# Kernel tuning notes

Measured on AMD Instinct MI355X. Metric: run time of the kernel, lower is better.

## Reference

```python
import jax, jax.numpy as jnp
import numpy as np

D_MODEL, N_HEADS, D_FF = 1024, 16, 4096
D_K = D_MODEL // N_HEADS
EPS = 1e-5


def setup_inputs() -> dict:
    key = jax.random.key(0)
    ks = jax.random.split(key, 16)
    s = 0.02
    p = {
        'x': jax.random.normal(ks[0], (2, 2048, D_MODEL), jnp.float32),
        'Wq': jax.random.normal(ks[1], (D_MODEL, D_MODEL), jnp.float32) * s,
        'bq': jnp.zeros((D_MODEL,), jnp.float32),
        'Wk': jax.random.normal(ks[2], (D_MODEL, D_MODEL), jnp.float32) * s,
        'bk': jnp.zeros((D_MODEL,), jnp.float32),
        'Wv': jax.random.normal(ks[3], (D_MODEL, D_MODEL), jnp.float32) * s,
        'bv': jnp.zeros((D_MODEL,), jnp.float32),
        'Wo': jax.random.normal(ks[4], (D_MODEL, D_MODEL), jnp.float32) * s,
        'bo': jnp.zeros((D_MODEL,), jnp.float32),
        'g1': jnp.ones((D_MODEL,), jnp.float32),
        'b1': jnp.zeros((D_MODEL,), jnp.float32),
        'W1': jax.random.normal(ks[5], (D_MODEL, D_FF), jnp.float32) * s,
        'bf1': jnp.zeros((D_FF,), jnp.float32),
        'W2': jax.random.normal(ks[6], (D_FF, D_MODEL), jnp.float32) * s,
        'bf2': jnp.zeros((D_MODEL,), jnp.float32),
        'g2': jnp.ones((D_MODEL,), jnp.float32),
        'b2': jnp.zeros((D_MODEL,), jnp.float32),
    }
    return p


def _layernorm(x, g, b):
    mu = jnp.mean(x, axis=-1, keepdims=True)
    var = jnp.var(x, axis=-1, keepdims=True)
    return (x - mu) * jax.lax.rsqrt(var + EPS) * g + b


def reference(x, Wq, bq, Wk, bk, Wv, bv, Wo, bo, g1, b1, W1, bf1, W2, bf2, g2, b2):
    B, S, _ = x.shape
    # project and split heads -> [B, H, S, d_k]
    def heads(y):
        return y.reshape(B, S, N_HEADS, D_K).transpose(0, 2, 1, 3)
    Q = heads(x @ Wq + bq)
    K = heads(x @ Wk + bk)
    V = heads(x @ Wv + bv)
    scores = jnp.einsum('bhqd,bhkd->bhqk', Q, K) / np.sqrt(D_K).astype(np.float32)
    attn = jax.nn.softmax(scores, axis=-1)  # dropout = identity (eval)
    ctx = jnp.einsum('bhqk,bhkd->bhqd', attn, V)
    ctx = ctx.transpose(0, 2, 1, 3).reshape(B, S, D_MODEL)
    attn_out = ctx @ Wo + bo
    h = _layernorm(x + attn_out, g1, b1)
    ff = (jax.nn.gelu(h @ W1 + bf1, approximate=False)) @ W2 + bf2
    out = _layernorm(h + ff, g2, b2)
    return out, attn
```

## Files before the change

kernel.cpp:

```cpp
#include <hip/hip_runtime.h>
#include <stdint.h>

#define SEQ 2048
#define BATCH 2
#define NH 16
#define DKH 64
#define DM 1024
#define DFF 4096
#define MTOT (BATCH*SEQ)

typedef __attribute__((ext_vector_type(8))) short bf16x8;
typedef __attribute__((ext_vector_type(4))) float f32x4;

__device__ __forceinline__ unsigned short f2bf(float f) {
  union { float f; unsigned u; } c; c.f = f;
  return (unsigned short)((c.u + 0x7fffu + ((c.u >> 16) & 1u)) >> 16);
}

__device__ __forceinline__ void gload_lds16(const void* g, void* l) {
  __builtin_amdgcn_global_load_lds((__attribute__((address_space(1))) unsigned int*)g,
                                   (__attribute__((address_space(3))) unsigned int*)l,
                                   16, 0, 0);
}


__global__ __launch_bounds__(256) void conv_bf16(const float* __restrict__ X,
                                                 unsigned short* __restrict__ O, int n) {
  const int i = blockIdx.x * 256 + threadIdx.x;
  const int idx = i * 4;
  if (idx >= n) return;
  const float4 f = *(const float4*)(X + idx);
  ushort4 u; u.x = f2bf(f.x); u.y = f2bf(f.y); u.z = f2bf(f.z); u.w = f2bf(f.w);
  *(ushort4*)(O + idx) = u;
}

__global__ __launch_bounds__(256) void trans_conv(const float* __restrict__ W,
                                                  unsigned short* __restrict__ Wt,
                                                  int K, int N) {
  __shared__ float t[32][33];
  const int n0 = blockIdx.x * 32, k0 = blockIdx.y * 32;
  const int tx = threadIdx.x & 31, ty = threadIdx.x >> 5;
#pragma unroll
  for (int i = 0; i < 4; ++i)
    t[ty + i * 8][tx] = W[(long)(k0 + ty + i * 8) * N + n0 + tx];
  __syncthreads();
#pragma unroll
  for (int i = 0; i < 4; ++i)
    Wt[(long)(n0 + ty + i * 8) * K + k0 + tx] = f2bf(t[tx][ty + i * 8]);
}

__global__ __launch_bounds__(256) void concat3(const float* __restrict__ a,
                                               const float* __restrict__ b,
                                               const float* __restrict__ c,
                                               float* __restrict__ o) {
  const int i = blockIdx.x * 256 + threadIdx.x;
  o[i] = i < 1024 ? a[i] : (i < 2048 ? b[i - 1024] : c[i - 2048]);
}

template <int EPI, int KS>
__global__ __launch_bounds__(256 * KS) void gemm_bt(
    const unsigned short* __restrict__ A, const unsigned short* __restrict__ Bt,
    float* __restrict__ Cf, unsigned short* __restrict__ Cbf,
    const float* __restrict__ bias, const float* __restrict__ resid,
    unsigned short* __restrict__ Vt,
    int M, int N, int K, int lda, int ldb, int ldc) {
  (void)M; (void)N;
  __shared__ unsigned short ldsAB[KS * 2 * 128 * 64];

  const int tid = threadIdx.x;
  const int ws = tid >> 8;
  const int t2 = tid & 255;
  const int lane = tid & 63;
  const int w4 = (tid >> 6) & 3;
  const int quad = lane >> 4, l16 = lane & 15;
  const int wm = (w4 >> 1) * 64, wn = (w4 & 1) * 64;
  const long tileM = (long)blockIdx.x * 128;
  const long tileN = (long)blockIdx.y * 128;

  unsigned short* ldsA = ldsAB + ws * 16384;
  unsigned short* ldsB = ldsA + 8192;
  const int kLen = K / KS;
  const int kBase = ws * kLen;

  const unsigned short* aS[4];
  const unsigned short* bS[4];
  int dOff[4];
#pragma unroll
  for (int it = 0; it < 4; ++it) {
    const int c = it * 256 + t2;
    const int slab = c >> 9, row = (c >> 2) & 127, q = c & 3;
    aS[it] = A  + (tileM + row) * (long)lda + kBase + slab * 32 + q * 8;
    bS[it] = Bt + (tileN + row) * (long)ldb + kBase + slab * 32 + q * 8;
    dOff[it] = c * 8;
  }

  f32x4 acc[4][4];
#pragma unroll
  for (int i = 0; i < 4; ++i)
#pragma unroll
    for (int j = 0; j < 4; ++j)
#pragma unroll
      for (int r = 0; r < 4; ++r) acc[i][j][r] = 0.f;

  for (int k0 = 0; k0 < kLen; k0 += 64) {
    __syncthreads();
#pragma unroll
    for (int it = 0; it < 4; ++it) {
      gload_lds16(aS[it] + k0, ldsA + dOff[it]);
      gload_lds16(bS[it] + k0, ldsB + dOff[it]);
    }
    __syncthreads();
#pragma unroll
    for (int s = 0; s < 2; ++s) {
      bf16x8 aF[4], bF[4];
#pragma unroll
      for (int i = 0; i < 4; ++i)
        aF[i] = *(const bf16x8*)&ldsA[(s * 128 + wm + i * 16 + l16) * 32 + quad * 8];
#pragma unroll
      for (int j = 0; j < 4; ++j)
        bF[j] = *(const bf16x8*)&ldsB[(s * 128 + wn + j * 16 + l16) * 32 + quad * 8];
#pragma unroll
      for (int i = 0; i < 4; ++i)
#pragma unroll
        for (int j = 0; j < 4; ++j)
          acc[i][j] = __builtin_amdgcn_mfma_f32_16x16x32_bf16(aF[i], bF[j], acc[i][j], 0, 0, 0);
    }
  }

  if constexpr (KS == 2) {
    __syncthreads();
    float* ldsF = (float*)ldsAB;
    if (ws == 1) {
#pragma unroll
      for (int i = 0; i < 4; ++i)
#pragma unroll
        for (int j = 0; j < 4; ++j)
#pragma unroll
          for (int r = 0; r < 4; ++r)
            ldsF[(wm + i * 16 + quad * 4 + r) * 128 + wn + j * 16 + l16] = acc[i][j][r];
    }
    __syncthreads();
    if (ws == 1) return;
#pragma unroll
    for (int i = 0; i < 4; ++i)
#pragma unroll
      for (int j = 0; j < 4; ++j)
#pragma unroll
        for (int r = 0; r < 4; ++r)
          acc[i][j][r] += ldsF[(wm + i * 16 + quad * 4 + r) * 128 + wn + j * 16 + l16];
  }

#pragma unroll
  for (int i = 0; i < 4; ++i) {
    const long mb = tileM + wm + i * 16 + quad * 4;
#pragma unroll
    for (int j = 0; j < 4; ++j) {
      const long n = tileN + wn + j * 16 + l16;
      const float bv = bias[n];
      if (EPI == 4) {
        if (n < 2048) {
          unsigned short* dst = Cbf + (n >> 10) * ((long)MTOT * DM);
          const int col = (int)n & 1023;
#pragma unroll
          for (int r = 0; r < 4; ++r)
            dst[(mb + r) * DM + col] = f2bf(acc[i][j][r] + bv);
        } else {
          const int nn = (int)n - 2048;
          const int bb2 = (int)(mb >> 11), s = (int)(mb & 2047);
          const int zz = bb2 * 16 + (nn >> 6);
          ushort4 u;
          u.x = f2bf(acc[i][j][0] + bv); u.y = f2bf(acc[i][j][1] + bv);
          u.z = f2bf(acc[i][j][2] + bv); u.w = f2bf(acc[i][j][3] + bv);
          *(ushort4*)&Vt[((long)zz * DKH + (nn & 63)) * SEQ + s] = u;
        }
      } else {
#pragma unroll
        for (int r = 0; r < 4; ++r) {
          const long m = mb + r;
          const long idx = m * ldc + n;
          const float v = acc[i][j][r];
          if (EPI == 0) {
            Cbf[idx] = f2bf(v + bv);
          } else if (EPI == 2) {
            Cf[idx] = v + bv + resid[idx];
          } else {
            const float tt = v + bv;
            Cbf[idx] = f2bf(0.5f * tt * (1.f + erff(tt * 0.70710678118654752f)));
          }
        }
      }
    }
  }
}

__device__ __forceinline__ void stage_k128(const unsigned short* __restrict__ gbase,
                                           unsigned short* lds, int tid) {
#pragma unroll
  for (int it = 0; it < 4; ++it) {
    const int c = it * 256 + tid;
    const int slab = c >> 9, row = (c >> 2) & 127, q = c & 3;
    gload_lds16(gbase + (long)row * DM + slab * 32 + q * 8, lds + c * 8);
  }
}
__device__ __forceinline__ void stage_v64(const unsigned short* __restrict__ gbase,
                                          unsigned short* lds, int tid) {
#pragma unroll
  for (int it = 0; it < 4; ++it) {
    const int c = it * 256 + tid;
    const int slab = c >> 8, row = (c >> 2) & 63, q = c & 3;
    gload_lds16(gbase + (long)row * SEQ + slab * 32 + q * 8, lds + c * 8);
  }
}

__global__ __launch_bounds__(256) void attn_all(const unsigned short* __restrict__ Qbf,
                                                const unsigned short* __restrict__ Kbf,
                                                const unsigned short* __restrict__ Vt,
                                                float* __restrict__ attn,
                                                unsigned short* __restrict__ Ctx) {
  const int z = blockIdx.z, b = z >> 4, h = z & 15;
  const int m0 = blockIdx.x * 128;

  __shared__ unsigned short ldsQ[2 * 128 * 32];
  __shared__ unsigned short ldsK[2 * 128 * 32];
  __shared__ unsigned short ldsV[4 * 64 * 32];
  __shared__ unsigned short ldsP[4 * 128 * 32];

  const int tid = threadIdx.x;
  const int lane = tid & 63, wave = tid >> 6;
  const int quad = lane >> 4, l16 = lane & 15;
  const int wm = (wave >> 1) * 64, wn = (wave & 1) * 64;
  const int wn2 = (wave & 1) * 32;

  const unsigned short* Qbase = Qbf + ((long)(b * SEQ + m0)) * DM + h * DKH;
  const unsigned short* Kz = Kbf + ((long)b * SEQ) * DM + h * DKH;
  const unsigned short* Vz = Vt + (long)z * DKH * SEQ;

  stage_k128(Qbase, ldsQ, tid);
  stage_k128(Kz, ldsK, tid);
  __syncthreads();

  bf16x8 qF[2][4];
#pragma unroll
  for (int s = 0; s < 2; ++s)
#pragma unroll
    for (int i = 0; i < 4; ++i)
      qF[s][i] = *(const bf16x8*)&ldsQ[(s * 128 + wm + i * 16 + l16) * 32 + quad * 8];
  __syncthreads();

  float rm[4][4], rl[4][4];
#pragma unroll
  for (int i = 0; i < 4; ++i)
#pragma unroll
    for (int r = 0; r < 4; ++r) { rm[i][r] = -1e30f; rl[i][r] = 0.f; }

  for (int n = 0; n < 16; ++n) {
    if (n) __syncthreads();
    if (n < 15) stage_k128(Kz + (long)(n + 1) * 128 * DM, (n & 1) ? ldsK : ldsQ, tid);
    const unsigned short* kc = (n & 1) ? ldsQ : ldsK;

    f32x4 acc[4][4];
#pragma unroll
    for (int i = 0; i < 4; ++i)
#pragma unroll
      for (int j = 0; j < 4; ++j)
#pragma unroll
        for (int r = 0; r < 4; ++r) acc[i][j][r] = 0.f;
#pragma unroll
    for (int s = 0; s < 2; ++s) {
      bf16x8 bF[4];
#pragma unroll
      for (int j = 0; j < 4; ++j)
        bF[j] = *(const bf16x8*)&kc[(s * 128 + wn + j * 16 + l16) * 32 + quad * 8];
#pragma unroll
      for (int i = 0; i < 4; ++i)
#pragma unroll
        for (int j = 0; j < 4; ++j)
          acc[i][j] = __builtin_amdgcn_mfma_f32_16x16x32_bf16(qF[s][i], bF[j], acc[i][j], 0, 0, 0);
    }
#pragma unroll
    for (int i = 0; i < 4; ++i)
#pragma unroll
      for (int r = 0; r < 4; ++r) {
        const float v0 = acc[i][0][r] * 0.125f, v1 = acc[i][1][r] * 0.125f;
        const float v2 = acc[i][2][r] * 0.125f, v3 = acc[i][3][r] * 0.125f;
        const float tm = fmaxf(fmaxf(v0, v1), fmaxf(v2, v3));
        const float mn = fmaxf(rm[i][r], tm);
        rl[i][r] = rl[i][r] * __expf(rm[i][r] - mn) +
                   __expf(v0 - mn) + __expf(v1 - mn) + __expf(v2 - mn) + __expf(v3 - mn);
        rm[i][r] = mn;
      }
  }

#pragma unroll
  for (int i = 0; i < 4; ++i)
#pragma unroll
    for (int r = 0; r < 4; ++r) {
      float m = rm[i][r], l = rl[i][r];
#pragma unroll
      for (int o = 1; o < 16; o <<= 1) {
        const float om = __shfl_xor(m, o), ol = __shfl_xor(l, o);
        const float mn = fmaxf(m, om);
        l = l * __expf(m - mn) + ol * __expf(om - mn);
        m = mn;
      }
      rm[i][r] = m; rl[i][r] = l;
    }

  float2* sm = (float2*)ldsP;
  if (l16 == 0) {
#pragma unroll
    for (int i = 0; i < 4; ++i)
#pragma unroll
      for (int r = 0; r < 4; ++r)
        sm[wave * 64 + i * 16 + quad * 4 + r] = make_float2(rm[i][r], rl[i][r]);
  }
  __syncthreads();
  float sM[4][4], sI[4][4];
#pragma unroll
  for (int i = 0; i < 4; ++i)
#pragma unroll
    for (int r = 0; r < 4; ++r) {
      const int rr = i * 16 + quad * 4 + r;
      const float2 A = sm[(wave & ~1) * 64 + rr];
      const float2 B = sm[((wave & ~1) + 1) * 64 + rr];
      const float M = fmaxf(A.x, B.x);
      const float Z = A.y * __expf(A.x - M) + B.y * __expf(B.x - M);
      sM[i][r] = M; sI[i][r] = 1.f / Z;
    }

  f32x4 acc_o[4][2];
#pragma unroll
  for (int i = 0; i < 4; ++i)
#pragma unroll
    for (int j = 0; j < 2; ++j)
#pragma unroll
      for (int r = 0; r < 4; ++r) acc_o[i][j][r] = 0.f;

  stage_k128(Kz, ldsK, tid);
  __syncthreads();

  for (int n = 0; n < 16; ++n) {
    if (n) __syncthreads();
    if (n < 15) stage_k128(Kz + (long)(n + 1) * 128 * DM, (n & 1) ? ldsK : ldsQ, tid);
    stage_v64(Vz + n * 128, ldsV, tid);
    const unsigned short* kc = (n & 1) ? ldsQ : ldsK;

    f32x4 acc[4][4];
#pragma unroll
    for (int i = 0; i < 4; ++i)
#pragma unroll
      for (int j = 0; j < 4; ++j)
#pragma unroll
        for (int r = 0; r < 4; ++r) acc[i][j][r] = 0.f;
    __builtin_amdgcn_s_setprio(1);
#pragma unroll
    for (int s = 0; s < 2; ++s) {
      bf16x8 bF[4];
#pragma unroll
      for (int j = 0; j < 4; ++j)
        bF[j] = *(const bf16x8*)&kc[(s * 128 + wn + j * 16 + l16) * 32 + quad * 8];
#pragma unroll
      for (int i = 0; i < 4; ++i)
#pragma unroll
        for (int j = 0; j < 4; ++j)
          acc[i][j] = __builtin_amdgcn_mfma_f32_16x16x32_bf16(qF[s][i], bF[j], acc[i][j], 0, 0, 0);
    }
    __builtin_amdgcn_s_setprio(0);

    float* attnBase = attn + (long)z * SEQ * SEQ + (long)m0 * SEQ + n * 128;
#pragma unroll
    for (int i = 0; i < 4; ++i)
#pragma unroll
      for (int r = 0; r < 4; ++r) {
        const int rowl = wm + i * 16 + quad * 4 + r;
        const float M = sM[i][r], I = sI[i][r];
#pragma unroll
        for (int j = 0; j < 4; ++j) {
          const int col = wn + j * 16 + l16;
          const float p = __expf(acc[i][j][r] * 0.125f - M) * I;
          attnBase[(long)rowl * SEQ + col] = p;
          ldsP[((col >> 5) * 128 + rowl) * 32 + (col & 31)] = f2bf(p);
        }
      }
    __syncthreads();

    __builtin_amdgcn_s_setprio(1);
#pragma unroll
    for (int slab = 0; slab < 4; ++slab) {
      bf16x8 aF[4], bF[2];
#pragma unroll
      for (int i = 0; i < 4; ++i)
        aF[i] = *(const bf16x8*)&ldsP[(slab * 128 + wm + i * 16 + l16) * 32 + quad * 8];
#pragma unroll
      for (int j = 0; j < 2; ++j)
        bF[j] = *(const bf16x8*)&ldsV[(slab * 64 + wn2 + j * 16 + l16) * 32 + quad * 8];
#pragma unroll
      for (int i = 0; i < 4; ++i)
#pragma unroll
        for (int j = 0; j < 2; ++j)
          acc_o[i][j] = __builtin_amdgcn_mfma_f32_16x16x32_bf16(aF[i], bF[j], acc_o[i][j], 0, 0, 0);
    }
    __builtin_amdgcn_s_setprio(0);
  }

#pragma unroll
  for (int i = 0; i < 4; ++i)
#pragma unroll
    for (int j = 0; j < 2; ++j) {
      const int d = h * DKH + wn2 + j * 16 + l16;
#pragma unroll
      for (int r = 0; r < 4; ++r) {
        const long m = (long)b * SEQ + m0 + wm + i * 16 + quad * 4 + r;
        Ctx[m * DM + d] = f2bf(acc_o[i][j][r]);
      }
    }
}

__global__ __launch_bounds__(256) void layernorm_row(const float* __restrict__ Y,
                                                     const float* __restrict__ g,
                                                     const float* __restrict__ bb,
                                                     float* __restrict__ outF,
                                                     unsigned short* __restrict__ outBf) {
  const long row = blockIdx.x;
  const float* p = Y + row * DM;
  const int tid = threadIdx.x;
  const float4 v = *(const float4*)(p + tid * 4);
  float s = v.x + v.y + v.z + v.w;
  float ss = v.x * v.x + v.y * v.y + v.z * v.z + v.w * v.w;
#pragma unroll
  for (int o = 32; o > 0; o >>= 1) { s += __shfl_xor(s, o); ss += __shfl_xor(ss, o); }
  __shared__ float rs[4], rss[4];
  if ((tid & 63) == 0) { rs[tid >> 6] = s; rss[tid >> 6] = ss; }
  __syncthreads();
  s = rs[0] + rs[1] + rs[2] + rs[3];
  ss = rss[0] + rss[1] + rss[2] + rss[3];
  const float mu = s * (1.f / DM);
  const float var = ss * (1.f / DM) - mu * mu;
  const float rstd = rsqrtf(var + 1e-5f);
  const float4 gv = *(const float4*)(g + tid * 4);
  const float4 bv = *(const float4*)(bb + tid * 4);
  float4 o;
  o.x = (v.x - mu) * rstd * gv.x + bv.x;
  o.y = (v.y - mu) * rstd * gv.y + bv.y;
  o.z = (v.z - mu) * rstd * gv.z + bv.z;
  o.w = (v.w - mu) * rstd * gv.w + bv.w;
  *(float4*)(outF + row * DM + tid * 4) = o;
  if (outBf) {
    ushort4 u; u.x = f2bf(o.x); u.y = f2bf(o.y); u.z = f2bf(o.z); u.w = f2bf(o.w);
    *(ushort4*)(outBf + row * DM + tid * 4) = u;
  }
}

extern "C" void kernel_launch(void* const* d_in, const int* in_sizes, int n_in,
                              void* d_out, int out_size, void* d_ws, size_t ws_size,
                              hipStream_t stream) {
  (void)in_sizes; (void)n_in; (void)out_size; (void)ws_size;
  const float* x  = (const float*)d_in[0];
  const float* Wq = (const float*)d_in[1];
  const float* bq = (const float*)d_in[2];
  const float* Wk = (const float*)d_in[3];
  const float* bk = (const float*)d_in[4];
  const float* Wv = (const float*)d_in[5];
  const float* bv = (const float*)d_in[6];
  const float* Wo = (const float*)d_in[7];
  const float* bo = (const float*)d_in[8];
  const float* g1 = (const float*)d_in[9];
  const float* b1 = (const float*)d_in[10];
  const float* W1 = (const float*)d_in[11];
  const float* bf1 = (const float*)d_in[12];
  const float* W2 = (const float*)d_in[13];
  const float* bf2 = (const float*)d_in[14];
  const float* g2 = (const float*)d_in[15];
  const float* b2 = (const float*)d_in[16];

  float* out  = (float*)d_out;
  float* attn = out + (long)MTOT * DM;

  char* w = (char*)d_ws;
  const long MB = 1024L * 1024L;
  unsigned short* Wqkvt = (unsigned short*)(w + 0 * MB);
  unsigned short* Wot   = (unsigned short*)(w + 6 * MB);
  unsigned short* W1t   = (unsigned short*)(w + 8 * MB);
  unsigned short* W2t   = (unsigned short*)(w + 16 * MB);
  unsigned short* xbf   = (unsigned short*)(w + 24 * MB);
  unsigned short* hbf   = xbf;
  unsigned short* Qbf   = (unsigned short*)(w + 32 * MB);
  unsigned short* Kbf   = (unsigned short*)(w + 40 * MB);
  unsigned short* Vt    = (unsigned short*)(w + 48 * MB);
  unsigned short* ctxbf = (unsigned short*)(w + 56 * MB);
  unsigned short* ffbf  = Qbf;
  float* bqkv = (float*)(w + 64 * MB);
  float* y    = (float*)(w + 64 * MB);
  float* h    = (float*)(w + 80 * MB);

  const dim3 blk(256), blk2(512);

  conv_bf16<<<dim3(MTOT * DM / 1024), blk, 0, stream>>>(x, xbf, MTOT * DM);
  trans_conv<<<dim3(DM / 32, DM / 32), blk, 0, stream>>>(Wq, Wqkvt, DM, DM);
  trans_conv<<<dim3(DM / 32, DM / 32), blk, 0, stream>>>(Wk, Wqkvt + 1024 * 1024, DM, DM);
  trans_conv<<<dim3(DM / 32, DM / 32), blk, 0, stream>>>(Wv, Wqkvt + 2 * 1024 * 1024, DM, DM);
  trans_conv<<<dim3(DM / 32, DM / 32), blk, 0, stream>>>(Wo, Wot, DM, DM);
  trans_conv<<<dim3(DFF / 32, DM / 32), blk, 0, stream>>>(W1, W1t, DM, DFF);
  trans_conv<<<dim3(DM / 32, DFF / 32), blk, 0, stream>>>(W2, W2t, DFF, DM);
  concat3<<<dim3(12), blk, 0, stream>>>(bq, bk, bv, bqkv);

  gemm_bt<4, 1><<<dim3(MTOT / 128, 3072 / 128), blk, 0, stream>>>(
      xbf, Wqkvt, nullptr, Qbf, bqkv, nullptr, Vt, MTOT, 3072, DM, DM, DM, DM);

  attn_all<<<dim3(SEQ / 128, 1, BATCH * NH), blk, 0, stream>>>(Qbf, Kbf, Vt, attn, ctxbf);

  gemm_bt<2, 2><<<dim3(MTOT / 128, DM / 128), blk2, 0, stream>>>(
      ctxbf, Wot, y, nullptr, bo, x, nullptr, MTOT, DM, DM, DM, DM, DM);
  layernorm_row<<<dim3(MTOT), blk, 0, stream>>>(y, g1, b1, h, hbf);

  gemm_bt<3, 1><<<dim3(MTOT / 128, DFF / 128), blk, 0, stream>>>(
      hbf, W1t, nullptr, ffbf, bf1, nullptr, nullptr, MTOT, DFF, DM, DM, DM, DFF);
  gemm_bt<2, 2><<<dim3(MTOT / 128, DM / 128), blk2, 0, stream>>>(
      ffbf, W2t, y, nullptr, bf2, h, nullptr, MTOT, DM, DFF, DFF, DFF, DM);
  layernorm_row<<<dim3(MTOT), blk, 0, stream>>>(y, g2, b2, out, nullptr);
}
```

Baseline: 970.5 us.

## Swizzle attention LDS tiles, transpose QK MFMA, vectorize nontemporal attn stores

New measurement: 948.5 us. -2.3%, faster.

```diff
diff --git a/kernel.cpp b/kernel.cpp
--- a/kernel.cpp
+++ b/kernel.cpp
@@ -22,6 +22,8 @@
                                    (__attribute__((address_space(3))) unsigned int*)l,
                                    16, 0, 0);
 }
+
+__device__ __forceinline__ int swz8(int row) { return ((row >> 1) & 3) * 8; }
 
 
 __global__ __launch_bounds__(256) void conv_bf16(const float* __restrict__ X,
@@ -198,8 +200,8 @@
 #pragma unroll
   for (int it = 0; it < 4; ++it) {
     const int c = it * 256 + tid;
-    const int slab = c >> 9, row = (c >> 2) & 127, q = c & 3;
-    gload_lds16(gbase + (long)row * DM + slab * 32 + q * 8, lds + c * 8);
+    const int slab = c >> 9, row = (c >> 2) & 127, q = (c & 3) * 8;
+    gload_lds16(gbase + (long)row * DM + slab * 32 + (q ^ swz8(row)), lds + c * 8);
   }
 }
 __device__ __forceinline__ void stage_v64(const unsigned short* __restrict__ gbase,
@@ -207,8 +209,8 @@
 #pragma unroll
   for (int it = 0; it < 4; ++it) {
     const int c = it * 256 + tid;
-    const int slab = c >> 8, row = (c >> 2) & 63, q = c & 3;
-    gload_lds16(gbase + (long)row * SEQ + slab * 32 + q * 8, lds + c * 8);
+    const int slab = c >> 8, row = (c >> 2) & 63, q = (c & 3) * 8;
+    gload_lds16(gbase + (long)row * SEQ + slab * 32 + (q ^ swz8(row)), lds + c * 8);
   }
 }
 
@@ -243,15 +245,15 @@
 #pragma unroll
   for (int s = 0; s < 2; ++s)
 #pragma unroll
-    for (int i = 0; i < 4; ++i)
-      qF[s][i] = *(const bf16x8*)&ldsQ[(s * 128 + wm + i * 16 + l16) * 32 + quad * 8];
+    for (int i = 0; i < 4; ++i) {
+      const int row = wm + i * 16 + l16;
+      qF[s][i] = *(const bf16x8*)&ldsQ[(s * 128 + row) * 32 + ((quad * 8) ^ swz8(row))];
+    }
   __syncthreads();
 
-  float rm[4][4], rl[4][4];
-#pragma unroll
-  for (int i = 0; i < 4; ++i)
-#pragma unroll
-    for (int r = 0; r < 4; ++r) { rm[i][r] = -1e30f; rl[i][r] = 0.f; }
+  float rm[4], rl[4];
+#pragma unroll
+  for (int i = 0; i < 4; ++i) { rm[i] = -1e30f; rl[i] = 0.f; }
 
   for (int n = 0; n < 16; ++n) {
     if (n) __syncthreads();
@@ -265,68 +267,73 @@
       for (int j = 0; j < 4; ++j)
 #pragma unroll
         for (int r = 0; r < 4; ++r) acc[i][j][r] = 0.f;
+    __builtin_amdgcn_s_setprio(1);
 #pragma unroll
     for (int s = 0; s < 2; ++s) {
       bf16x8 bF[4];
 #pragma unroll
+      for (int j = 0; j < 4; ++j) {
+        const int row = wn + j * 16 + l16;
+        bF[j] = *(const bf16x8*)&kc[(s * 128 + row) * 32 + ((quad * 8) ^ swz8(row))];
+      }
+#pragma unroll
+      for (int i = 0; i < 4; ++i)
+#pragma unroll
+        for (int j = 0; j < 4; ++j)
+          acc[i][j] = __builtin_amdgcn_mfma_f32_16x16x32_bf16(bF[j], qF[s][i], acc[i][j], 0, 0, 0);
+    }
+    __builtin_amdgcn_s_setprio(0);
+
+#pragma unroll
+    for (int i = 0; i < 4; ++i) {
+      float tm = acc[i][0][0];
+#pragma unroll
       for (int j = 0; j < 4; ++j)
-        bF[j] = *(const bf16x8*)&kc[(s * 128 + wn + j * 16 + l16) * 32 + quad * 8];
-#pragma unroll
-      for (int i = 0; i < 4; ++i)
-#pragma unroll
-        for (int j = 0; j < 4; ++j)
-          acc[i][j] = __builtin_amdgcn_mfma_f32_16x16x32_bf16(qF[s][i], bF[j], acc[i][j], 0, 0, 0);
-    }
+#pragma unroll
+        for (int r = 0; r < 4; ++r) tm = fmaxf(tm, acc[i][j][r]);
+      const float tms = tm * 0.125f;
+      const float mn = fmaxf(rm[i], tms);
+      float sum = 0.f;
+#pragma unroll
+      for (int j = 0; j < 4; ++j)
+#pragma unroll
+        for (int r = 0; r < 4; ++r)
+          sum += __expf(fmaf(acc[i][j][r], 0.125f, -mn));
+      rl[i] = rl[i] * __expf(rm[i] - mn) + sum;
+      rm[i] = mn;
+    }
+  }
+
+#pragma unroll
+  for (int i = 0; i < 4; ++i) {
+    float m = rm[i], l = rl[i];
+#pragma unroll
+    for (int o = 16; o < 64; o <<= 1) {
+      const float om = __shfl_xor(m, o), ol = __shfl_xor(l, o);
+      const float mn = fmaxf(m, om);
+      l = l * __expf(m - mn) + ol * __expf(om - mn);
+      m = mn;
+    }
+    rm[i] = m; rl[i] = l;
+  }
+
+  float2* sm = (float2*)ldsP;
+  if (quad == 0) {
 #pragma unroll
     for (int i = 0; i < 4; ++i)
-#pragma unroll
-      for (int r = 0; r < 4; ++r) {
-        const float v0 = acc[i][0][r] * 0.125f, v1 = acc[i][1][r] * 0.125f;
-        const float v2 = acc[i][2][r] * 0.125f, v3 = acc[i][3][r] * 0.125f;
-        const float tm = fmaxf(fmaxf(v0, v1), fmaxf(v2, v3));
-        const float mn = fmaxf(rm[i][r], tm);
-        rl[i][r] = rl[i][r] * __expf(rm[i][r] - mn) +
-                   __expf(v0 - mn) + __expf(v1 - mn) + __expf(v2 - mn) + __expf(v3 - mn);
-        rm[i][r] = mn;
-      }
-  }
-
-#pragma unroll
-  for (int i = 0; i < 4; ++i)
-#pragma unroll
-    for (int r = 0; r < 4; ++r) {
-      float m = rm[i][r], l = rl[i][r];
-#pragma unroll
-      for (int o = 1; o < 16; o <<= 1) {
-        const float om = __shfl_xor(m, o), ol = __shfl_xor(l, o);
-        const float mn = fmaxf(m, om);
-        l = l * __expf(m - mn) + ol * __expf(om - mn);
-        m = mn;
-      }
-      rm[i][r] = m; rl[i][r] = l;
-    }
-
-  float2* sm = (float2*)ldsP;
-  if (l16 == 0) {
-#pragma unroll
-    for (int i = 0; i < 4; ++i)
-#pragma unroll
-      for (int r = 0; r < 4; ++r)
-        sm[wave * 64 + i * 16 + quad * 4 + r] = make_float2(rm[i][r], rl[i][r]);
+      sm[wave * 64 + i * 16 + l16] = make_float2(rm[i], rl[i]);
   }
   __syncthreads();
-  float sM[4][4], sI[4][4];
-#pragma unroll
-  for (int i = 0; i < 4; ++i)
-#pragma unroll
-    for (int r = 0; r < 4; ++r) {
-      const int rr = i * 16 + quad * 4 + r;
-      const float2 A = sm[(wave & ~1) * 64 + rr];
-      const float2 B = sm[((wave & ~1) + 1) * 64 + rr];
-      const float M = fmaxf(A.x, B.x);
-      const float Z = A.y * __expf(A.x - M) + B.y * __expf(B.x - M);
-      sM[i][r] = M; sI[i][r] = 1.f / Z;
-    }
+  float sM[4], sI[4];
+#pragma unroll
+  for (int i = 0; i < 4; ++i) {
+    const int rr = i * 16 + l16;
+    const float2 A = sm[(wave & ~1) * 64 + rr];
+    const float2 B = sm[((wave & ~1) + 1) * 64 + rr];
+    const float M = fmaxf(A.x, B.x);
+    const float Z = A.y * __expf(A.x - M) + B.y * __expf(B.x - M);
+    sM[i] = M; sI[i] = 1.f / Z;
+  }
 
   f32x4 acc_o[4][2];
 #pragma unroll
@@ -357,31 +364,38 @@
     for (int s = 0; s < 2; ++s) {
       bf16x8 bF[4];
 #pragma unroll
-      for (int j = 0; j < 4; ++j)
-        bF[j] = *(const bf16x8*)&kc[(s * 128 + wn + j * 16 + l16) * 32 + quad * 8];
+      for (int j = 0; j < 4; ++j) {
+        const int row = wn + j * 16 + l16;
+        bF[j] = *(const bf16x8*)&kc[(s * 128 + row) * 32 + ((quad * 8) ^ swz8(row))];
+      }
 #pragma unroll
       for (int i = 0; i < 4; ++i)
 #pragma unroll
         for (int j = 0; j < 4; ++j)
-          acc[i][j] = __builtin_amdgcn_mfma_f32_16x16x32_bf16(qF[s][i], bF[j], acc[i][j], 0, 0, 0);
+          acc[i][j] = __builtin_amdgcn_mfma_f32_16x16x32_bf16(bF[j], qF[s][i], acc[i][j], 0, 0, 0);
     }
     __builtin_amdgcn_s_setprio(0);
 
     float* attnBase = attn + (long)z * SEQ * SEQ + (long)m0 * SEQ + n * 128;
 #pragma unroll
-    for (int i = 0; i < 4; ++i)
-#pragma unroll
-      for (int r = 0; r < 4; ++r) {
-        const int rowl = wm + i * 16 + quad * 4 + r;
-        const float M = sM[i][r], I = sI[i][r];
-#pragma unroll
-        for (int j = 0; j < 4; ++j) {
-          const int col = wn + j * 16 + l16;
-          const float p = __expf(acc[i][j][r] * 0.125f - M) * I;
-          attnBase[(long)rowl * SEQ + col] = p;
-          ldsP[((col >> 5) * 128 + rowl) * 32 + (col & 31)] = f2bf(p);
-        }
-      }
+    for (int i = 0; i < 4; ++i) {
+      const int rowl = wm + i * 16 + l16;
+      const float M = sM[i], I = sI[i];
+#pragma unroll
+      for (int j = 0; j < 4; ++j) {
+        const int col = wn + j * 16 + quad * 4;
+        f32x4 p4;
+        p4[0] = __expf(fmaf(acc[i][j][0], 0.125f, -M)) * I;
+        p4[1] = __expf(fmaf(acc[i][j][1], 0.125f, -M)) * I;
+        p4[2] = __expf(fmaf(acc[i][j][2], 0.125f, -M)) * I;
+        p4[3] = __expf(fmaf(acc[i][j][3], 0.125f, -M)) * I;
+        __builtin_nontemporal_store(p4, (f32x4*)(attnBase + (long)rowl * SEQ + col));
+        ushort4 u;
+        u.x = f2bf(p4[0]); u.y = f2bf(p4[1]); u.z = f2bf(p4[2]); u.w = f2bf(p4[3]);
+        const int uoff = ((col >> 5) * 128 + rowl) * 32 + ((col & 31) ^ swz8(rowl));
+        *(ushort4*)&ldsP[uoff] = u;
+      }
+    }
     __syncthreads();
 
     __builtin_amdgcn_s_setprio(1);
@@ -389,11 +403,15 @@
     for (int slab = 0; slab < 4; ++slab) {
       bf16x8 aF[4], bF[2];
 #pragma unroll
-      for (int i = 0; i < 4; ++i)
-        aF[i] = *(const bf16x8*)&ldsP[(slab * 128 + wm + i * 16 + l16) * 32 + quad * 8];
-#pragma unroll
-      for (int j = 0; j < 2; ++j)
-        bF[j] = *(const bf16x8*)&ldsV[(slab * 64 + wn2 + j * 16 + l16) * 32 + quad * 8];
+      for (int i = 0; i < 4; ++i) {
+        const int row = wm + i * 16 + l16;
+        aF[i] = *(const bf16x8*)&ldsP[(slab * 128 + row) * 32 + ((quad * 8) ^ swz8(row))];
+      }
+#pragma unroll
+      for (int j = 0; j < 2; ++j) {
+        const int d = wn2 + j * 16 + l16;
+        bF[j] = *(const bf16x8*)&ldsV[(slab * 64 + d) * 32 + ((quad * 8) ^ swz8(d))];
+      }
 #pragma unroll
       for (int i = 0; i < 4; ++i)
 #pragma unroll
```
